# Kernel tuning notes

Measured on AMD Instinct MI355X. Metric: run time of the kernel, lower is better.

Reference implementation:

```python
import jax, jax.numpy as jnp
import numpy as np
from jax import lax

BN_EPS = 1e-5


def setup_inputs() -> dict:
    key = jax.random.key(0)
    ks = jax.random.split(key, 3)
    B, N, D = 96, 20, 2048
    return {
        "x": jax.random.normal(ks[0], (B, N, D), dtype=jnp.float32),
        "conv_w": jax.random.normal(ks[1], (D, 2 * D), dtype=jnp.float32) * 0.02,
        "conv_b": jax.random.normal(ks[2], (D,), dtype=jnp.float32) * 0.02,
        "bn_gamma": jnp.ones((D,), dtype=jnp.float32),
        "bn_beta": jnp.zeros((D,), dtype=jnp.float32),
        "bn_mean": jnp.zeros((D,), dtype=jnp.float32),
        "bn_var": jnp.ones((D,), dtype=jnp.float32),
        "n_neighbor": 10,
    }


def reference(x, conv_w, conv_b, bn_gamma, bn_beta, bn_mean, bn_var, n_neighbor):
    # x: [B, N, D] -> xt: [B, D, N] (channels-first point cloud of view features)
    xt = jnp.transpose(x, (0, 2, 1))
    B, D, N = xt.shape
    k = int(n_neighbor)

    # pairwise squared distances: [B, N, N]
    sq = jnp.sum(xt * xt, axis=1, keepdims=True)            # [B, 1, N]
    inner = jnp.einsum("bdn,bdm->bnm", xt, xt)              # [B, N, N]
    adj = sq + (-2.0) * inner + jnp.transpose(sq, (0, 2, 1))

    # k nearest neighbors (smallest distance) -> idx [B, N, k]
    _, nn_idx = lax.top_k(-adj, k)

    # gather neighbor features without the O(N^2) expand: [B, D, N, k]
    neighbors = jax.vmap(lambda xb, idx: xb[:, idx])(xt, nn_idx)

    center = xt[:, :, :, None]                              # [B, D, N, 1]
    edge = jnp.concatenate(
        [jnp.broadcast_to(center, (B, D, N, k)), neighbors - center], axis=1
    )                                                       # [B, 2D, N, k]

    # 1x1 conv (GEMM over channel dim) + BatchNorm (inference) + ReLU
    y = jnp.einsum("oc,bcnk->bonk", conv_w, edge) + conv_b[None, :, None, None]
    inv = bn_gamma / jnp.sqrt(bn_var + BN_EPS)
    y = y * inv[None, :, None, None] + (bn_beta - bn_mean * inv)[None, :, None, None]
    y = jax.nn.relu(y)

    # max over neighbors, then max over points -> [B, D, 1, 1]
    y = jnp.max(y, axis=-1, keepdims=True)
    y = jnp.max(y, axis=2, keepdims=True)
    return y
```

## Files before the change

### kernel.cpp

```cpp
#include <hip/hip_runtime.h>
#include <hip/hip_bf16.h>
#include <math.h>

#define BN_EPS 1e-5f
#define B_  96
#define N_  20
#define D_  2048
#define K_  10
#define M_  (B_*N_)
#define R_  (2*D_)

typedef __attribute__((ext_vector_type(8))) short bf16x8;
typedef __attribute__((ext_vector_type(4))) float f32x4;
typedef __attribute__((ext_vector_type(8))) unsigned short ushort8;

static __device__ __forceinline__ unsigned short f2bf(float f) {
  unsigned int u = __builtin_bit_cast(unsigned int, f);
  u = u + 0x7fffu + ((u >> 16) & 1u);
  return (unsigned short)(u >> 16);
}

#define GLOAD_LDS16(g, l) \
  __builtin_amdgcn_global_load_lds((const __attribute__((address_space(1))) void*)(g), \
                                   (__attribute__((address_space(3))) void*)(l), 16, 0, 0)

__global__ __launch_bounds__(512) void prep_kernel(const float* __restrict__ x,
                                                   const float* __restrict__ cw,
                                                   int* __restrict__ nn_idx,
                                                   unsigned short* __restrict__ Xb,
                                                   unsigned short* __restrict__ Wn)
{
  int t = threadIdx.x;
  if (blockIdx.x >= B_) {
    int cb = blockIdx.x - B_;
    for (int i = cb*512 + t; i < R_*D_/8; i += 416*512) {
      int r = i >> 8;
      int k = (i & 255) * 8;
      const float* src = cw + (size_t)(r >> 1) * R_ + ((r & 1) << 11) + k;
      float4 a = *(const float4*)src, c = *(const float4*)(src + 4);
      ushort8 o = { f2bf(a.x), f2bf(a.y), f2bf(a.z), f2bf(a.w),
                    f2bf(c.x), f2bf(c.y), f2bf(c.z), f2bf(c.w) };
      *((ushort8*)Wn + i) = o;
    }
    return;
  }
  int b = blockIdx.x, w = t >> 6, lane = t & 63;
  __shared__ float innr[N_*N_];
  __shared__ float adjl[N_*N_];
  const float* xb = x + (size_t)b * N_ * D_;
  int rows[3] = { w, 15 - w, (w < 4) ? 16 + w : -1 };
  #pragma unroll
  for (int ri = 0; ri < 3; ++ri) {
    int n = rows[ri];
    if (n < 0) continue;
    const float4* xnp = (const float4*)(xb + n * D_);
    float4 xn[8];
    #pragma unroll
    for (int j = 0; j < 8; ++j) xn[j] = xnp[lane + 64*j];
    for (int m = n; m < N_; ++m) {
      const float4* xmp = (const float4*)(xb + m * D_);
      float s0 = 0.f, s1 = 0.f, s2 = 0.f, s3 = 0.f;
      #pragma unroll
      for (int j = 0; j < 8; ++j) {
        float4 v = xmp[lane + 64*j];
        float d = fmaf(xn[j].x, v.x, fmaf(xn[j].y, v.y,
                  fmaf(xn[j].z, v.z, xn[j].w * v.w)));
        if      ((j&3)==0) s0 += d;
        else if ((j&3)==1) s1 += d;
        else if ((j&3)==2) s2 += d;
        else               s3 += d;
      }
      float s = (s0 + s1) + (s2 + s3);
      #pragma unroll
      for (int off = 32; off > 0; off >>= 1)
        s += __shfl_xor(s, off, 64);
      if (lane == 0) { innr[n*N_+m] = s; innr[m*N_+n] = s; }
    }
  }
  __syncthreads();
  for (int p = t; p < N_*N_; p += 512) {
    int n = p / N_, m = p % N_;
    adjl[p] = innr[n*N_+n] + innr[m*N_+m] - 2.f * innr[p];
  }
  __syncthreads();
  if (t < N_) {
    int n = t;
    unsigned mask = 0;
    for (int it = 0; it < K_; ++it) {
      float bv = INFINITY; int bi = 0;
      for (int m = 0; m < N_; ++m) {
        if (!((mask >> m) & 1u)) {
          float v = adjl[n*N_+m];
          if (v < bv) { bv = v; bi = m; }
        }
      }
      mask |= 1u << bi;
      nn_idx[(b*N_ + n)*K_ + it] = bi;
    }
  }
  unsigned short* xo = Xb + (size_t)b * N_ * D_;
  for (int i = t; i < N_*D_/8; i += 512) {
    const float4* src = (const float4*)xb + (size_t)i * 2;
    float4 a = src[0], c = src[1];
    ushort8 o = { f2bf(a.x), f2bf(a.y), f2bf(a.z), f2bf(a.w),
                  f2bf(c.x), f2bf(c.y), f2bf(c.z), f2bf(c.w) };
    *((ushort8*)xo + i) = o;
  }
}

__global__ __launch_bounds__(256, 3) void fused_gemm(
    const unsigned short* __restrict__ Xb, const unsigned short* __restrict__ Wn,
    const int* __restrict__ nn_idx, const float* __restrict__ conv_b,
    const float* __restrict__ gamma, const float* __restrict__ beta,
    const float* __restrict__ mean, const float* __restrict__ var,
    float* __restrict__ out)
{
  __shared__ __align__(16) char smem[53248];
  float* Cl  = (float*)smem;
  int*   idxl = (int*)(smem + 40960);

  int flat = blockIdx.y * 24 + blockIdx.x;
  int nf = (flat & 7) * 96 + (flat >> 3);
  int bx = nf % 24, by = nf / 24;

  int t = threadIdx.x, lane = t & 63, w = t >> 6;
  int m0 = bx * 80, b0 = bx * 4;
  int r0 = by * 128, o0 = by * 64;
  int rowsel = lane & 15, ksel = lane >> 4;

  f32x4 acc[5][2] = {};

  auto stage = [&](int sel, int k0) {
    unsigned short* Asb = (unsigned short*)(smem + sel*26624);
    unsigned short* Bsb = (unsigned short*)(smem + sel*26624 + 10240);
    #pragma unroll
    for (int i = 0; i < 3; ++i) {
      int fl = i*256 + t;
      if (fl < 640) {
        int row = fl >> 3, kc = fl & 7;
        GLOAD_LDS16(Xb + (size_t)(m0 + row) * D_ + k0 + ((kc ^ (row & 7)) << 3),
                    Asb + fl*8);
      }
    }
    #pragma unroll
    for (int i = 0; i < 4; ++i) {
      int fl = i*256 + t;
      int row = fl >> 3, kc = fl & 7;
      GLOAD_LDS16(Wn + (size_t)(r0 + row) * D_ + k0 + ((kc ^ (row & 7)) << 3),
                  Bsb + fl*8);
    }
  };

  auto compute = [&](int sel) {
    unsigned short* Asb = (unsigned short*)(smem + sel*26624);
    unsigned short* Bsb = (unsigned short*)(smem + sel*26624 + 10240);
    #pragma unroll
    for (int ks = 0; ks < 2; ++ks) {
      int swz = ((ks*4 + ksel) ^ (rowsel & 7)) << 3;
      bf16x8 a[5], bfr[2];
      #pragma unroll
      for (int mi = 0; mi < 5; ++mi)
        a[mi] = *(const bf16x8*)(Asb + (mi*16 + rowsel)*64 + swz);
      #pragma unroll
      for (int ri = 0; ri < 2; ++ri)
        bfr[ri] = *(const bf16x8*)(Bsb + (w*32 + ri*16 + rowsel)*64 + swz);
      #pragma unroll
      for (int mi = 0; mi < 5; ++mi)
        #pragma unroll
        for (int ri = 0; ri < 2; ++ri)
          acc[mi][ri] = __builtin_amdgcn_mfma_f32_16x16x32_bf16(a[mi], bfr[ri], acc[mi][ri], 0, 0, 0);
    }
  };

  stage(0, 0);
  for (int kt = 0; kt < D_/64; ++kt) {
    __syncthreads();
    if (kt + 1 < D_/64) stage((kt+1) & 1, (kt+1)*64);
    compute(kt & 1);
  }
  __syncthreads();

  #pragma unroll
  for (int mi = 0; mi < 5; ++mi)
    #pragma unroll
    for (int ri = 0; ri < 2; ++ri)
      #pragma unroll
      for (int rg = 0; rg < 4; ++rg)
        Cl[(mi*16 + ksel*4 + rg)*128 + w*32 + ri*16 + rowsel] = acc[mi][ri][rg];
  for (int i = t; i < 4*N_*K_; i += 256) idxl[i] = nn_idx[b0*N_*K_ + i];
  __syncthreads();

  int bb = w, oo = lane;
  int og = o0 + oo;
  float invv  = gamma[og] / sqrtf(var[og] + BN_EPS);
  float shift = fmaf(-mean[og], invv, beta[og]);
  float bias  = conv_b[og];
  float best = 0.f;
  int rbase = bb * N_;
  for (int n = 0; n < N_; ++n) {
    float Pv = Cl[(rbase + n)*128 + oo*2];
    float Qn = Cl[(rbase + n)*128 + oo*2 + 1];
    float aa = Pv - Qn + bias;
    const int* ix = idxl + bb*N_*K_ + n*K_;
    #pragma unroll
    for (int kk = 0; kk < K_; ++kk) {
      int j = ix[kk];
      float v = fmaf(aa + Cl[(rbase + j)*128 + oo*2 + 1], invv, shift);
      best = fmaxf(best, v);
    }
  }
  out[(size_t)(b0 + bb) * D_ + og] = best;
}

extern "C" void kernel_launch(void* const* d_in, const int* in_sizes, int n_in,
                              void* d_out, int out_size, void* d_ws, size_t ws_size,
                              hipStream_t stream)
{
  const float* x      = (const float*)d_in[0];
  const float* conv_w = (const float*)d_in[1];
  const float* conv_b = (const float*)d_in[2];
  const float* gamma  = (const float*)d_in[3];
  const float* beta   = (const float*)d_in[4];
  const float* mean   = (const float*)d_in[5];
  const float* var    = (const float*)d_in[6];

  int* nn_idx = (int*)d_ws;
  unsigned short* Xb = (unsigned short*)((char*)d_ws + 76800);
  unsigned short* Wn = (unsigned short*)((char*)d_ws + 76800 + (size_t)M_*D_*2);

  prep_kernel<<<512, 512, 0, stream>>>(x, conv_w, nn_idx, Xb, Wn);
  fused_gemm<<<dim3(24, 32), 256, 0, stream>>>(
      Xb, Wn, nn_idx, conv_b, gamma, beta, mean, var, (float*)d_out);
}
```

Baseline: 77.63 us.

## Split prep into per-row inner-product kernel and separate top-k kernel

The prep kernel is split in two. The first computes pairwise inner products with one wavefront per (batch, row) task across 240 blocks, writes them to global memory, and uses 512 other blocks to convert both x and the weights to bf16. A small second kernel builds the distances and runs the top-k selection per batch. This spreads the distance work over many more CUs than the previous one-block-per-batch design, at the cost of an extra launch and a global round trip for the inner-product matrix.

```diff
diff --git a/kernel.cpp b/kernel.cpp
--- a/kernel.cpp
+++ b/kernel.cpp
@@ -24,63 +24,72 @@
   __builtin_amdgcn_global_load_lds((const __attribute__((address_space(1))) void*)(g), \
                                    (__attribute__((address_space(3))) void*)(l), 16, 0, 0)
 
-__global__ __launch_bounds__(512) void prep_kernel(const float* __restrict__ x,
-                                                   const float* __restrict__ cw,
-                                                   int* __restrict__ nn_idx,
-                                                   unsigned short* __restrict__ Xb,
-                                                   unsigned short* __restrict__ Wn)
+__global__ __launch_bounds__(512, 2) void prep1_kernel(const float* __restrict__ x,
+                                                       const float* __restrict__ cw,
+                                                       float* __restrict__ innr_g,
+                                                       unsigned short* __restrict__ Xb,
+                                                       unsigned short* __restrict__ Wn)
 {
   int t = threadIdx.x;
-  if (blockIdx.x >= B_) {
-    int cb = blockIdx.x - B_;
-    for (int i = cb*512 + t; i < R_*D_/8; i += 416*512) {
-      int r = i >> 8;
-      int k = (i & 255) * 8;
-      const float* src = cw + (size_t)(r >> 1) * R_ + ((r & 1) << 11) + k;
-      float4 a = *(const float4*)src, c = *(const float4*)(src + 4);
-      ushort8 o = { f2bf(a.x), f2bf(a.y), f2bf(a.z), f2bf(a.w),
-                    f2bf(c.x), f2bf(c.y), f2bf(c.z), f2bf(c.w) };
-      *((ushort8*)Wn + i) = o;
+  if (blockIdx.x >= 240) {
+    for (int i = (blockIdx.x - 240)*512 + t; i < 1540096; i += 512*512) {
+      if (i < 491520) {
+        const float* src = x + (size_t)i * 8;
+        float4 a = *(const float4*)src, c = *(const float4*)(src + 4);
+        ushort8 o = { f2bf(a.x), f2bf(a.y), f2bf(a.z), f2bf(a.w),
+                      f2bf(c.x), f2bf(c.y), f2bf(c.z), f2bf(c.w) };
+        *((ushort8*)Xb + i) = o;
+      } else {
+        int j = i - 491520;
+        int r = j >> 8, k = (j & 255) * 8;
+        const float* src = cw + (size_t)(r >> 1) * R_ + ((r & 1) << 11) + k;
+        float4 a = *(const float4*)src, c = *(const float4*)(src + 4);
+        ushort8 o = { f2bf(a.x), f2bf(a.y), f2bf(a.z), f2bf(a.w),
+                      f2bf(c.x), f2bf(c.y), f2bf(c.z), f2bf(c.w) };
+        *((ushort8*)Wn + j) = o;
+      }
     }
     return;
   }
-  int b = blockIdx.x, w = t >> 6, lane = t & 63;
-  __shared__ float innr[N_*N_];
+  int w = t >> 6, lane = t & 63;
+  int task = blockIdx.x * 8 + w;
+  int b = task / N_, n = task % N_;
+  const float* xb = x + (size_t)b * N_ * D_;
+  const float4* pn = (const float4*)(xb + n * D_);
+  float4 c[8];
+  #pragma unroll
+  for (int j = 0; j < 8; ++j) c[j] = pn[lane + 64*j];
+  float* ig = innr_g + b * (N_*N_);
+  for (int m = n; m < N_; ++m) {
+    const float4* pm = (const float4*)(xb + m * D_);
+    float s0 = 0.f, s1 = 0.f, s2 = 0.f, s3 = 0.f;
+    #pragma unroll
+    for (int j = 0; j < 8; ++j) {
+      float4 v = pm[lane + 64*j];
+      float d = fmaf(c[j].x, v.x, fmaf(c[j].y, v.y,
+                fmaf(c[j].z, v.z, c[j].w * v.w)));
+      if      ((j&3)==0) s0 += d;
+      else if ((j&3)==1) s1 += d;
+      else if ((j&3)==2) s2 += d;
+      else               s3 += d;
+    }
+    float s = (s0 + s1) + (s2 + s3);
+    #pragma unroll
+    for (int off = 32; off > 0; off >>= 1)
+      s += __shfl_xor(s, off, 64);
+    if (lane == 0) { ig[n*N_ + m] = s; ig[m*N_ + n] = s; }
+  }
+}
+
+__global__ __launch_bounds__(64) void topk_kernel(const float* __restrict__ innr_g,
+                                                  int* __restrict__ nn_idx)
+{
+  int b = blockIdx.x, t = threadIdx.x;
   __shared__ float adjl[N_*N_];
-  const float* xb = x + (size_t)b * N_ * D_;
-  int rows[3] = { w, 15 - w, (w < 4) ? 16 + w : -1 };
-  #pragma unroll
-  for (int ri = 0; ri < 3; ++ri) {
-    int n = rows[ri];
-    if (n < 0) continue;
-    const float4* xnp = (const float4*)(xb + n * D_);
-    float4 xn[8];
-    #pragma unroll
-    for (int j = 0; j < 8; ++j) xn[j] = xnp[lane + 64*j];
-    for (int m = n; m < N_; ++m) {
-      const float4* xmp = (const float4*)(xb + m * D_);
-      float s0 = 0.f, s1 = 0.f, s2 = 0.f, s3 = 0.f;
-      #pragma unroll
-      for (int j = 0; j < 8; ++j) {
-        float4 v = xmp[lane + 64*j];
-        float d = fmaf(xn[j].x, v.x, fmaf(xn[j].y, v.y,
-                  fmaf(xn[j].z, v.z, xn[j].w * v.w)));
-        if      ((j&3)==0) s0 += d;
-        else if ((j&3)==1) s1 += d;
-        else if ((j&3)==2) s2 += d;
-        else               s3 += d;
-      }
-      float s = (s0 + s1) + (s2 + s3);
-      #pragma unroll
-      for (int off = 32; off > 0; off >>= 1)
-        s += __shfl_xor(s, off, 64);
-      if (lane == 0) { innr[n*N_+m] = s; innr[m*N_+n] = s; }
-    }
-  }
-  __syncthreads();
-  for (int p = t; p < N_*N_; p += 512) {
+  const float* ig = innr_g + b * (N_*N_);
+  for (int p = t; p < N_*N_; p += 64) {
     int n = p / N_, m = p % N_;
-    adjl[p] = innr[n*N_+n] + innr[m*N_+m] - 2.f * innr[p];
+    adjl[p] = ig[n*N_+n] + ig[m*N_+m] - 2.f * ig[p];
   }
   __syncthreads();
   if (t < N_) {
@@ -98,14 +107,6 @@
       nn_idx[(b*N_ + n)*K_ + it] = bi;
     }
   }
-  unsigned short* xo = Xb + (size_t)b * N_ * D_;
-  for (int i = t; i < N_*D_/8; i += 512) {
-    const float4* src = (const float4*)xb + (size_t)i * 2;
-    float4 a = src[0], c = src[1];
-    ushort8 o = { f2bf(a.x), f2bf(a.y), f2bf(a.z), f2bf(a.w),
-                  f2bf(c.x), f2bf(c.y), f2bf(c.z), f2bf(c.w) };
-    *((ushort8*)xo + i) = o;
-  }
 }
 
 __global__ __launch_bounds__(256, 3) void fused_gemm(
@@ -227,8 +228,10 @@
   int* nn_idx = (int*)d_ws;
   unsigned short* Xb = (unsigned short*)((char*)d_ws + 76800);
   unsigned short* Wn = (unsigned short*)((char*)d_ws + 76800 + (size_t)M_*D_*2);
-
-  prep_kernel<<<512, 512, 0, stream>>>(x, conv_w, nn_idx, Xb, Wn);
+  float* innr_g = (float*)((char*)d_ws + 76800 + (size_t)M_*D_*2 + (size_t)R_*D_*2);
+
+  prep1_kernel<<<752, 512, 0, stream>>>(x, conv_w, innr_g, Xb, Wn);
+  topk_kernel<<<B_, 64, 0, stream>>>(innr_g, nn_idx);
   fused_gemm<<<dim3(24, 32), 256, 0, stream>>>(
       Xb, Wn, nn_idx, conv_b, gamma, beta, mean, var, (float*)d_out);
 }
```

After: 99.20 us. 1.28x slower.
